# Optimization experiments

Hardware: AMD Instinct MI355X
Metric: run time of the kernel (lower is better)

The kernel has to match this reference:

```python
import jax, jax.numpy as jnp
import numpy as np
import math

EMBED = 1024
HEADS = 16
HEAD_DIM = EMBED // HEADS


def setup_inputs() -> dict:
    key = jax.random.key(0)
    k1, k2, k3 = jax.random.split(key, 3)
    B, C, N = 2, EMBED, 2048
    x = jax.random.normal(k1, (B, C, N), dtype=jnp.float32)
    # Conv1d(kernel_size=1, bias=False) weights, stored as [out_ch, in_ch]
    fan = 1.0 / math.sqrt(EMBED)
    w_qkv = jax.random.uniform(k2, (3 * EMBED, EMBED), dtype=jnp.float32, minval=-fan, maxval=fan)
    w_out = jax.random.uniform(k3, (EMBED, EMBED), dtype=jnp.float32, minval=-fan, maxval=fan)
    return {"x": x, "w_qkv": w_qkv, "w_out": w_out}


def reference(x, w_qkv, w_out):
    B, C, N = x.shape
    H, HD = HEADS, HEAD_DIM
    # 1x1 conv == channel matmul: [B, 3E, N]
    qkv = jnp.einsum('oc,bcn->bon', w_qkv, x)
    # permute -> [B, N, 3E]; reshape splits 3E as (H, 3*HD) per original code
    qkv = qkv.transpose(0, 2, 1).reshape(B, N, H, 3 * HD)
    qkv = qkv.transpose(0, 2, 1, 3)  # [B, H, N, 3*HD]
    q, k, v = jnp.split(qkv, 3, axis=-1)  # each [B, H, N, HD]
    scale = 1.0 / math.sqrt(HD)
    scores = jnp.einsum('bhnd,bhmd->bhnm', q, k) * scale
    weight = jax.nn.softmax(scores, axis=-1)
    vals = jnp.einsum('bhnm,bhmd->bhnd', weight, v)
    vals = vals.transpose(0, 2, 1, 3).reshape(B, N, C)  # [B, N, C]
    y = jnp.einsum('oc,bnc->bon', w_out, vals)  # [B, C, N]
    return y
```

## Files before the change

kernel.cpp:

```cpp
#include <hip/hip_runtime.h>
#include <stdint.h>

typedef unsigned short u16;
typedef __attribute__((ext_vector_type(8))) short bf16x8;
typedef __attribute__((ext_vector_type(4))) float f32x4;

#define NSEQ  2048
#define EMBED 1024
#define NHEAD 16
#define HDIM  64
#define QSCALE 0.1803368801111204f

__device__ __forceinline__ u16 f2bf(float f) {
  uint32_t u = __builtin_bit_cast(uint32_t, f);
  u += 0x7fffu + ((u >> 16) & 1u);
  return (u16)(u >> 16);
}

__device__ __forceinline__ uint32_t cvtpk(float a, float b) {
  uint32_t r;
  asm("v_cvt_pk_bf16_f32 %0, %1, %2" : "=v"(r) : "v"(a), "v"(b));
  return r;
}

__device__ __forceinline__ void gl_lds16(const void* g, void* l) {
  __builtin_amdgcn_global_load_lds(
      (const __attribute__((address_space(1))) void*)g,
      (__attribute__((address_space(3))) void*)l, 16, 0, 0);
}

struct alignas(8) us4 { u16 a, b, c, d; };

__global__ __launch_bounds__(256)
void convertw(const float* __restrict__ wq, const float* __restrict__ wo,
              u16* __restrict__ oq, u16* __restrict__ oo) {
  int idx = blockIdx.x * 256 + threadIdx.x;
  const float* src;
  u16* dst;
  if (idx < 786432) { src = wq; dst = oq; }
  else { idx -= 786432; src = wo; dst = oo; }
  f32x4 v = ((const f32x4*)src)[idx];
  us4 r;
  r.a = f2bf(v[0]); r.b = f2bf(v[1]); r.c = f2bf(v[2]); r.d = f2bf(v[3]);
  ((us4*)dst)[idx] = r;
}

__global__ __launch_bounds__(256)
void transpose_x(const float* __restrict__ x, u16* __restrict__ xT) {
  __shared__ float tile[32][33];
  const int b = blockIdx.z;
  const int n0 = blockIdx.x * 32, c0 = blockIdx.y * 32;
  const int tx = threadIdx.x & 31, ty = threadIdx.x >> 5;
  const float* xb = x + (size_t)b * EMBED * NSEQ;
  #pragma unroll
  for (int k = 0; k < 4; ++k)
    tile[ty + k * 8][tx] = xb[(size_t)(c0 + ty + k * 8) * NSEQ + n0 + tx];
  __syncthreads();
  u16* xTb = xT + (size_t)b * NSEQ * EMBED;
  #pragma unroll
  for (int k = 0; k < 4; ++k)
    xTb[(size_t)(n0 + ty + k * 8) * EMBED + c0 + tx] = f2bf(tile[tx][ty + k * 8]);
}

template<int EPI, int MR>
__global__ __launch_bounds__(256, 2)
void gemm_bt(const u16* __restrict__ A, const u16* __restrict__ Bm,
             u16* __restrict__ o_q, u16* __restrict__ o_k, u16* __restrict__ o_vt,
             float* __restrict__ o_f)
{
  __shared__ u16 lA[MR * 32 * 64];
  __shared__ u16 lB[128 * 64];
  const int t  = threadIdx.x;
  const int w  = t >> 6;
  const int l  = t & 63;
  const int lr = l & 15, lh = l >> 4;
  const int wm = w >> 1, wn = w & 1;
  const int bz = blockIdx.z;
  const int NT  = (EPI == 0 ? 384 : 256);
  const int c   = blockIdx.x + 16 * blockIdx.y;
  const int swz = (c & 7) * (NT / 8) + (c >> 3);
  const int m0  = (swz & 15) * (MR * 32);
  const int n0  = (swz >> 4) * 128;

  const u16* Ab = A  + (EPI == 0 ? (size_t)bz * NSEQ * EMBED : (size_t)0);
  const u16* Bb = Bm + (EPI == 0 ? (size_t)0 : (size_t)bz * NSEQ * EMBED);

  f32x4 acc[MR][4];
  #pragma unroll
  for (int i = 0; i < MR; ++i)
    #pragma unroll
    for (int j = 0; j < 4; ++j)
      acc[i][j] = (f32x4){0.f, 0.f, 0.f, 0.f};

  const int srow = t >> 3;
  const int slot = t & 7;
  char* ldsA = (char*)lA + (w << 10);
  char* ldsB = (char*)lB + (w << 10);

  for (int k0 = 0; k0 < EMBED; k0 += 64) {
    __syncthreads();
    #pragma unroll
    for (int i = 0; i < MR; ++i) {
      const int row = i * 32 + srow;
      const int sc  = ((slot * 16) ^ ((row & 7) << 4)) >> 1;
      gl_lds16(Ab + (size_t)(m0 + row) * EMBED + k0 + sc, ldsA + i * 4096);
    }
    #pragma unroll
    for (int i = 0; i < 4; ++i) {
      const int row = i * 32 + srow;
      const int sc  = ((slot * 16) ^ ((row & 7) << 4)) >> 1;
      gl_lds16(Bb + (size_t)(n0 + row) * EMBED + k0 + sc, ldsB + i * 4096);
    }
    __syncthreads();
    #pragma unroll
    for (int kk = 0; kk < 2; ++kk) {
      bf16x8 af[MR], bfr[4];
      #pragma unroll
      for (int mr = 0; mr < MR; ++mr) {
        const int row = wm * (MR * 16) + mr * 16 + lr;
        const int c2  = (kk * 64 + lh * 16) ^ ((row & 7) << 4);
        af[mr] = *(const bf16x8*)((const char*)lA + row * 128 + c2);
      }
      #pragma unroll
      for (int nc = 0; nc < 4; ++nc) {
        const int row = wn * 64 + nc * 16 + lr;
        const int c2  = (kk * 64 + lh * 16) ^ ((row & 7) << 4);
        bfr[nc] = *(const bf16x8*)((const char*)lB + row * 128 + c2);
      }
      #pragma unroll
      for (int mr = 0; mr < MR; ++mr)
        #pragma unroll
        for (int nc = 0; nc < 4; ++nc)
          acc[mr][nc] = __builtin_amdgcn_mfma_f32_16x16x32_bf16(
              af[mr], bfr[nc], acc[mr][nc], 0, 0, 0);
    }
  }

  if constexpr (EPI == 0) {
    #pragma unroll
    for (int mr = 0; mr < MR; ++mr) {
      #pragma unroll
      for (int nc = 0; nc < 4; ++nc) {
        const int o  = n0 + wn * 64 + nc * 16 + lr;
        const int h  = o / 192;
        const int rr = o - h * 192;
        const size_t bh = (size_t)bz * NHEAD + h;
        #pragma unroll
        for (int r = 0; r < 4; ++r) {
          const int n = m0 + wm * (MR * 16) + mr * 16 + lh * 4 + r;
          if (rr < 64)       o_q [(bh * NSEQ + n) * HDIM + rr]         = f2bf(acc[mr][nc][r] * QSCALE);
          else if (rr < 128) o_k [(bh * NSEQ + n) * HDIM + (rr - 64)]  = f2bf(acc[mr][nc][r]);
          else               o_vt[(bh * HDIM + (rr - 128)) * NSEQ + n] = f2bf(acc[mr][nc][r]);
        }
      }
    }
  } else {
    #pragma unroll
    for (int mr = 0; mr < MR; ++mr)
      #pragma unroll
      for (int nc = 0; nc < 4; ++nc)
        #pragma unroll
        for (int r = 0; r < 4; ++r) {
          const int o = m0 + wm * (MR * 16) + mr * 16 + lh * 4 + r;
          const int n = n0 + wn * 64 + nc * 16 + lr;
          o_f[((size_t)bz * EMBED + o) * NSEQ + n] = acc[mr][nc][r];
        }
  }
}

__global__ __launch_bounds__(256, 4)
void attn(const u16* __restrict__ Q, const u16* __restrict__ K,
          const u16* __restrict__ Vt, u16* __restrict__ vals)
{
  __shared__ u16 lK[2][64 * 64], lV[2][64 * 64], lQP[64 * 64];
  const int t  = threadIdx.x;
  const int w  = t >> 6, l = t & 63;
  const int lr = l & 15, lh = l >> 4;
  const int bid = blockIdx.x;
  const int s   = bid >> 3;
  const int bh  = (bid & 7) + 8 * (s >> 5);
  const int q0  = (s & 31) * 64;
  const int b  = bh >> 4, h = bh & 15;
  const size_t qk0 = (size_t)bh * NSEQ * HDIM;
  const size_t vt0 = (size_t)bh * HDIM * NSEQ;
  const int srow = t >> 3, slot = t & 7;
  const int swzr = (lr & 7) << 4;
  char* const pbase = (char*)lQP + (w << 11) + lr * 128;

#define STAGE(J, KB, VB) do {                                                  \
    _Pragma("unroll")                                                          \
    for (int i_ = 0; i_ < 2; ++i_) {                                           \
      const int row_ = i_ * 32 + srow;                                         \
      const int sc_  = ((slot * 16) ^ ((row_ & 7) << 4)) >> 1;                 \
      gl_lds16(K  + qk0 + (size_t)((J) + row_) * HDIM + sc_,                   \
               (char*)(KB) + i_ * 4096 + (w << 10));                           \
      gl_lds16(Vt + vt0 + (size_t)row_ * NSEQ + (J) + sc_,                     \
               (char*)(VB) + i_ * 4096 + (w << 10));                           \
    }                                                                          \
  } while (0)

#define ATILE(KB, VB) do {                                                     \
    f32x4 accS[4];                                                             \
    _Pragma("unroll")                                                          \
    for (int f_ = 0; f_ < 4; ++f_) accS[f_] = (f32x4){0.f, 0.f, 0.f, 0.f};     \
    __builtin_amdgcn_s_setprio(1);                                             \
    _Pragma("unroll")                                                          \
    for (int kk_ = 0; kk_ < 2; ++kk_)                                          \
      _Pragma("unroll")                                                        \
      for (int f_ = 0; f_ < 4; ++f_) {                                         \
        const int row_ = f_ * 16 + lr;                                         \
        const int c2_  = (kk_ * 64 + lh * 16) ^ swzr;                          \
        bf16x8 kf_ = *(const bf16x8*)((const char*)(KB) + row_ * 128 + c2_);   \
        accS[f_] = __builtin_amdgcn_mfma_f32_16x16x32_bf16(kf_, qf[kk_],       \
                                                           accS[f_], 0, 0, 0);\
      }                                                                        \
    __builtin_amdgcn_s_setprio(0);                                             \
    float fm0_ = fmaxf(fmaxf(accS[0][0], accS[0][1]), fmaxf(accS[0][2], accS[0][3])); \
    float fm1_ = fmaxf(fmaxf(accS[1][0], accS[1][1]), fmaxf(accS[1][2], accS[1][3])); \
    float fm2_ = fmaxf(fmaxf(accS[2][0], accS[2][1]), fmaxf(accS[2][2], accS[2][3])); \
    float fm3_ = fmaxf(fmaxf(accS[3][0], accS[3][1]), fmaxf(accS[3][2], accS[3][3])); \
    float tm_ = fmaxf(fmaxf(fm0_, fm1_), fmaxf(fm2_, fm3_));                   \
    tm_ = fmaxf(tm_, __shfl_xor(tm_, 16, 64));                                 \
    tm_ = fmaxf(tm_, __shfl_xor(tm_, 32, 64));                                 \
    if (tm_ > m + 8.f) {            \
      const float al_ = exp2f(m - tm_);                                        \
      lsum *= al_;                                                             \
      _Pragma("unroll")                                                        \
      for (int fd_ = 0; fd_ < 4; ++fd_)                                        \
        _Pragma("unroll")                                                      \
        for (int r_ = 0; r_ < 4; ++r_) accO[fd_][r_] *= al_;                   \
      m = tm_;                                                                 \
    }                                                                          \
    _Pragma("unroll")                                                          \
    for (int f_ = 0; f_ < 4; ++f_) {                                           \
      const float e0_ = exp2f(accS[f_][0] - m);                                \
      const float e1_ = exp2f(accS[f_][1] - m);                                \
      const float e2_ = exp2f(accS[f_][2] - m);                                \
      const float e3_ = exp2f(accS[f_][3] - m);                                \
      lsum += (e0_ + e1_) + (e2_ + e3_);   \
      uint2 pw_;                                                               \
      pw_.x = cvtpk(e0_, e1_);                                                 \
      pw_.y = cvtpk(e2_, e3_);                                                 \
      *(uint2*)(pbase + ((f_ * 32 + lh * 8) ^ swzr)) = pw_;                    \
    }                                                                          \
    __builtin_amdgcn_s_setprio(1);                                             \
    _Pragma("unroll")                                                          \
    for (int kk_ = 0; kk_ < 2; ++kk_) {                                        \
      bf16x8 pf_ = *(const bf16x8*)(pbase + ((kk_ * 64 + lh * 16) ^ swzr));    \
      _Pragma("unroll")                                                        \
      for (int fd_ = 0; fd_ < 4; ++fd_) {                                      \
        const int row_ = fd_ * 16 + lr;                                        \
        const int c2_  = (kk_ * 64 + lh * 16) ^ swzr;                          \
        bf16x8 vf_ = *(const bf16x8*)((const char*)(VB) + row_ * 128 + c2_);   \
        accO[fd_] = __builtin_amdgcn_mfma_f32_16x16x32_bf16(vf_, pf_,          \
                                                            accO[fd_], 0, 0, 0);\
      }                                                                        \
    }                                                                          \
    __builtin_amdgcn_s_setprio(0);                                             \
  } while (0)

  #pragma unroll
  for (int i = 0; i < 2; ++i) {
    const int row = i * 32 + srow;
    const int sc  = ((slot * 16) ^ ((row & 7) << 4)) >> 1;
    gl_lds16(Q + qk0 + (size_t)(q0 + row) * HDIM + sc,
             (char*)lQP + i * 4096 + (w << 10));
  }
  STAGE(0, lK[0], lV[0]);
  STAGE(64, lK[1], lV[1]);
  __syncthreads();

  bf16x8 qf[2];
  {
    const int qrow = w * 16 + lr;
    #pragma unroll
    for (int kk = 0; kk < 2; ++kk)
      qf[kk] = *(const bf16x8*)((const char*)lQP + qrow * 128 +
                                ((kk * 64 + lh * 16) ^ ((qrow & 7) << 4)));
  }

  f32x4 accO[4];
  #pragma unroll
  for (int i = 0; i < 4; ++i) accO[i] = (f32x4){0.f, 0.f, 0.f, 0.f};
  float m = -1e30f, lsum = 0.f;

  for (int tt = 0; tt < 15; ++tt) {
    const int j0 = tt * 128;
    ATILE(lK[0], lV[0]);
    __syncthreads();
    STAGE(j0 + 128, lK[0], lV[0]);
    ATILE(lK[1], lV[1]);
    __syncthreads();
    STAGE(j0 + 192, lK[1], lV[1]);
  }
  ATILE(lK[0], lV[0]);
  __syncthreads();
  ATILE(lK[1], lV[1]);

  lsum += __shfl_xor(lsum, 16, 64);
  lsum += __shfl_xor(lsum, 32, 64);
  const float rl = 1.0f / lsum;
  const int n = q0 + w * 16 + lr;
  #pragma unroll
  for (int fd = 0; fd < 4; ++fd) {
    uint2 ow;
    ow.x = cvtpk(accO[fd][0] * rl, accO[fd][1] * rl);
    ow.y = cvtpk(accO[fd][2] * rl, accO[fd][3] * rl);
    const int c = h * HDIM + fd * 16 + lh * 4;
    *(uint2*)(vals + ((size_t)b * NSEQ + n) * EMBED + c) = ow;
  }
#undef STAGE
#undef ATILE
}

extern "C" void kernel_launch(void* const* d_in, const int* in_sizes, int n_in,
                              void* d_out, int out_size, void* d_ws, size_t ws_size,
                              hipStream_t stream) {
  const float* x    = (const float*)d_in[0];
  const float* wqkv = (const float*)d_in[1];
  const float* wout = (const float*)d_in[2];
  float* y = (float*)d_out;
  char* ws = (char*)d_ws;

  u16* b_wqkv = (u16*)(ws);
  u16* b_wout = (u16*)(ws + 6291456);
  u16* b_xT   = (u16*)(ws + 8388608);
  u16* b_Q    = (u16*)(ws + 16777216);
  u16* b_K    = (u16*)(ws + 25165824);
  u16* b_Vt   = (u16*)(ws + 33554432);
  u16* b_vals = (u16*)(ws + 41943040);

  convertw<<<4096, 256, 0, stream>>>(wqkv, wout, b_wqkv, b_wout);
  transpose_x<<<dim3(64, 32, 2), 256, 0, stream>>>(x, b_xT);
  gemm_bt<0, 4><<<dim3(16, 24, 2), 256, 0, stream>>>(b_xT, b_wqkv, b_Q, b_K, b_Vt, nullptr);
  attn<<<1024, 256, 0, stream>>>(b_Q, b_K, b_Vt, b_vals);
  gemm_bt<1, 2><<<dim3(16, 16, 2), 256, 0, stream>>>(b_wout, b_vals, nullptr, nullptr, nullptr, y);
}
```

Baseline: 200.2 us.

## Precompute LDS addresses, use raw v_exp_f32, wave-uniform rescale, raise GEMM occupancy

After: 189.1 us. 5.5% less time.

```diff
diff --git a/kernel.cpp b/kernel.cpp
--- a/kernel.cpp
+++ b/kernel.cpp
@@ -20,6 +20,12 @@
 __device__ __forceinline__ uint32_t cvtpk(float a, float b) {
   uint32_t r;
   asm("v_cvt_pk_bf16_f32 %0, %1, %2" : "=v"(r) : "v"(a), "v"(b));
+  return r;
+}
+
+__device__ __forceinline__ float ex2f(float x) {
+  float r;
+  asm("v_exp_f32 %0, %1" : "=v"(r) : "v"(x));
   return r;
 }
 
@@ -63,7 +69,7 @@
 }
 
 template<int EPI, int MR>
-__global__ __launch_bounds__(256, 2)
+__global__ __launch_bounds__(256, (MR == 4 ? 3 : 4))
 void gemm_bt(const u16* __restrict__ A, const u16* __restrict__ Bm,
              u16* __restrict__ o_q, u16* __restrict__ o_k, u16* __restrict__ o_vt,
              float* __restrict__ o_f)
@@ -94,39 +100,38 @@
 
   const int srow = t >> 3;
   const int slot = t & 7;
-  char* ldsA = (char*)lA + (w << 10);
-  char* ldsB = (char*)lB + (w << 10);
-
-  for (int k0 = 0; k0 < EMBED; k0 += 64) {
+  const int sc   = ((slot * 16) ^ ((srow & 7) << 4)) >> 1;
+  const int swzr = (lr & 7) << 4;
+
+  const char* aRd0 = (const char*)lA + (wm * (MR * 16) + lr) * 128 + ((lh * 16) ^ swzr);
+  const char* aRd1 = (const char*)lA + (wm * (MR * 16) + lr) * 128 + ((64 + lh * 16) ^ swzr);
+  const char* bRd0 = (const char*)lB + (wn * 64 + lr) * 128 + ((lh * 16) ^ swzr);
+  const char* bRd1 = (const char*)lB + (wn * 64 + lr) * 128 + ((64 + lh * 16) ^ swzr);
+  char* const aDst = (char*)lA + (w << 10);
+  char* const bDst = (char*)lB + (w << 10);
+  const u16* aP = Ab + (size_t)(m0 + srow) * EMBED + sc;
+  const u16* bP = Bb + (size_t)(n0 + srow) * EMBED + sc;
+
+  for (int k0 = 0; k0 < 16; ++k0) {
     __syncthreads();
     #pragma unroll
-    for (int i = 0; i < MR; ++i) {
-      const int row = i * 32 + srow;
-      const int sc  = ((slot * 16) ^ ((row & 7) << 4)) >> 1;
-      gl_lds16(Ab + (size_t)(m0 + row) * EMBED + k0 + sc, ldsA + i * 4096);
-    }
-    #pragma unroll
-    for (int i = 0; i < 4; ++i) {
-      const int row = i * 32 + srow;
-      const int sc  = ((slot * 16) ^ ((row & 7) << 4)) >> 1;
-      gl_lds16(Bb + (size_t)(n0 + row) * EMBED + k0 + sc, ldsB + i * 4096);
-    }
+    for (int i = 0; i < MR; ++i)
+      gl_lds16(aP + (size_t)i * 32 * EMBED, aDst + i * 4096);
+    #pragma unroll
+    for (int i = 0; i < 4; ++i)
+      gl_lds16(bP + (size_t)i * 32 * EMBED, bDst + i * 4096);
     __syncthreads();
     #pragma unroll
     for (int kk = 0; kk < 2; ++kk) {
+      const char* aRk = kk ? aRd1 : aRd0;
+      const char* bRk = kk ? bRd1 : bRd0;
       bf16x8 af[MR], bfr[4];
       #pragma unroll
-      for (int mr = 0; mr < MR; ++mr) {
-        const int row = wm * (MR * 16) + mr * 16 + lr;
-        const int c2  = (kk * 64 + lh * 16) ^ ((row & 7) << 4);
-        af[mr] = *(const bf16x8*)((const char*)lA + row * 128 + c2);
-      }
-      #pragma unroll
-      for (int nc = 0; nc < 4; ++nc) {
-        const int row = wn * 64 + nc * 16 + lr;
-        const int c2  = (kk * 64 + lh * 16) ^ ((row & 7) << 4);
-        bfr[nc] = *(const bf16x8*)((const char*)lB + row * 128 + c2);
-      }
+      for (int mr = 0; mr < MR; ++mr)
+        af[mr] = *(const bf16x8*)(aRk + mr * 2048);
+      #pragma unroll
+      for (int nc = 0; nc < 4; ++nc)
+        bfr[nc] = *(const bf16x8*)(bRk + nc * 2048);
       #pragma unroll
       for (int mr = 0; mr < MR; ++mr)
         #pragma unroll
@@ -134,6 +139,7 @@
           acc[mr][nc] = __builtin_amdgcn_mfma_f32_16x16x32_bf16(
               af[mr], bfr[nc], acc[mr][nc], 0, 0, 0);
     }
+    aP += 64; bP += 64;
   }
 
   if constexpr (EPI == 0) {
@@ -172,7 +178,7 @@
 void attn(const u16* __restrict__ Q, const u16* __restrict__ K,
           const u16* __restrict__ Vt, u16* __restrict__ vals)
 {
-  __shared__ u16 lK[2][64 * 64], lV[2][64 * 64], lQP[64 * 64];
+  __shared__ u16 sm[5 * 64 * 64];
   const int t  = threadIdx.x;
   const int w  = t >> 6, l = t & 63;
   const int lr = l & 15, lh = l >> 4;
@@ -184,36 +190,47 @@
   const size_t qk0 = (size_t)bh * NSEQ * HDIM;
   const size_t vt0 = (size_t)bh * HDIM * NSEQ;
   const int srow = t >> 3, slot = t & 7;
+  const int sc   = ((slot * 16) ^ ((srow & 7) << 4)) >> 1;
   const int swzr = (lr & 7) << 4;
-  char* const pbase = (char*)lQP + (w << 11) + lr * 128;
-
-#define STAGE(J, KB, VB) do {                                                  \
+
+  char* const smB  = (char*)sm;
+  char* const stD  = smB + (w << 10);
+  const char* kv0  = smB + lr * 128 + ((lh * 16) ^ swzr);
+  const char* kv1  = smB + lr * 128 + ((64 + lh * 16) ^ swzr);
+  const char* kvp0 = kv0 + 32768 + (w << 11);
+  const char* kvp1 = kv1 + 32768 + (w << 11);
+  char* const pwb  = smB + 32768 + (w << 11) + lr * 128;
+  char* const pw_[4] = { pwb + ((0 + lh * 8) ^ swzr),  pwb + ((32 + lh * 8) ^ swzr),
+                         pwb + ((64 + lh * 8) ^ swzr),  pwb + ((96 + lh * 8) ^ swzr) };
+
+  const u16* kP = K  + qk0 + (size_t)srow * HDIM + sc;
+  const u16* vP = Vt + vt0 + (size_t)srow * NSEQ + sc;
+
+#define STAGE(KOFF, VOFF, TB) do {                                             \
     _Pragma("unroll")                                                          \
     for (int i_ = 0; i_ < 2; ++i_) {                                           \
-      const int row_ = i_ * 32 + srow;                                         \
-      const int sc_  = ((slot * 16) ^ ((row_ & 7) << 4)) >> 1;                 \
-      gl_lds16(K  + qk0 + (size_t)((J) + row_) * HDIM + sc_,                   \
-               (char*)(KB) + i_ * 4096 + (w << 10));                           \
-      gl_lds16(Vt + vt0 + (size_t)row_ * NSEQ + (J) + sc_,                     \
-               (char*)(VB) + i_ * 4096 + (w << 10));                           \
+      gl_lds16(kP + (KOFF) + (size_t)i_ * 32 * HDIM,                           \
+               stD + (TB) * 8192 + i_ * 4096);                                 \
+      gl_lds16(vP + (VOFF) + (size_t)i_ * 32 * NSEQ,                           \
+               stD + 16384 + (TB) * 8192 + i_ * 4096);                         \
     }                                                                          \
   } while (0)
 
-#define ATILE(KB, VB) do {                                                     \
+#define ATILE(TB) do {                                                         \
     f32x4 accS[4];                                                             \
     _Pragma("unroll")                                                          \
     for (int f_ = 0; f_ < 4; ++f_) accS[f_] = (f32x4){0.f, 0.f, 0.f, 0.f};     \
     __builtin_amdgcn_s_setprio(1);                                             \
     _Pragma("unroll")                                                          \
-    for (int kk_ = 0; kk_ < 2; ++kk_)                                          \
+    for (int kk_ = 0; kk_ < 2; ++kk_) {                                        \
+      const char* kvk_ = kk_ ? kv1 : kv0;                                      \
       _Pragma("unroll")                                                        \
       for (int f_ = 0; f_ < 4; ++f_) {                                         \
-        const int row_ = f_ * 16 + lr;                                         \
-        const int c2_  = (kk_ * 64 + lh * 16) ^ swzr;                          \
-        bf16x8 kf_ = *(const bf16x8*)((const char*)(KB) + row_ * 128 + c2_);   \
+        bf16x8 kf_ = *(const bf16x8*)(kvk_ + (TB) * 8192 + f_ * 2048);         \
         accS[f_] = __builtin_amdgcn_mfma_f32_16x16x32_bf16(kf_, qf[kk_],       \
                                                            accS[f_], 0, 0, 0);\
       }                                                                        \
+    }                                                                          \
     __builtin_amdgcn_s_setprio(0);                                             \
     float fm0_ = fmaxf(fmaxf(accS[0][0], accS[0][1]), fmaxf(accS[0][2], accS[0][3])); \
     float fm1_ = fmaxf(fmaxf(accS[1][0], accS[1][1]), fmaxf(accS[1][2], accS[1][3])); \
@@ -222,36 +239,36 @@
     float tm_ = fmaxf(fmaxf(fm0_, fm1_), fmaxf(fm2_, fm3_));                   \
     tm_ = fmaxf(tm_, __shfl_xor(tm_, 16, 64));                                 \
     tm_ = fmaxf(tm_, __shfl_xor(tm_, 32, 64));                                 \
-    if (tm_ > m + 8.f) {            \
-      const float al_ = exp2f(m - tm_);                                        \
+    if (__any(tm_ - m > 8.f)) {                    \
+      const float nm_ = fmaxf(m, tm_);                                         \
+      const float al_ = ex2f(m - nm_);         \
       lsum *= al_;                                                             \
       _Pragma("unroll")                                                        \
       for (int fd_ = 0; fd_ < 4; ++fd_)                                        \
         _Pragma("unroll")                                                      \
         for (int r_ = 0; r_ < 4; ++r_) accO[fd_][r_] *= al_;                   \
-      m = tm_;                                                                 \
+      m = nm_;                                                                 \
     }                                                                          \
     _Pragma("unroll")                                                          \
     for (int f_ = 0; f_ < 4; ++f_) {                                           \
-      const float e0_ = exp2f(accS[f_][0] - m);                                \
-      const float e1_ = exp2f(accS[f_][1] - m);                                \
-      const float e2_ = exp2f(accS[f_][2] - m);                                \
-      const float e3_ = exp2f(accS[f_][3] - m);                                \
-      lsum += (e0_ + e1_) + (e2_ + e3_);   \
-      uint2 pw_;                                                               \
-      pw_.x = cvtpk(e0_, e1_);                                                 \
-      pw_.y = cvtpk(e2_, e3_);                                                 \
-      *(uint2*)(pbase + ((f_ * 32 + lh * 8) ^ swzr)) = pw_;                    \
+      const float e0_ = ex2f(accS[f_][0] - m);                                 \
+      const float e1_ = ex2f(accS[f_][1] - m);                                 \
+      const float e2_ = ex2f(accS[f_][2] - m);                                 \
+      const float e3_ = ex2f(accS[f_][3] - m);                                 \
+      lsum += (e0_ + e1_) + (e2_ + e3_);                 \
+      uint2 pw_v;                                                              \
+      pw_v.x = cvtpk(e0_, e1_);                                                \
+      pw_v.y = cvtpk(e2_, e3_);                                                \
+      *(uint2*)(pw_[f_]) = pw_v;                                               \
     }                                                                          \
     __builtin_amdgcn_s_setprio(1);                                             \
     _Pragma("unroll")                                                          \
     for (int kk_ = 0; kk_ < 2; ++kk_) {                                        \
-      bf16x8 pf_ = *(const bf16x8*)(pbase + ((kk_ * 64 + lh * 16) ^ swzr));    \
+      const char* kvk_ = kk_ ? kv1 : kv0;                                      \
+      bf16x8 pf_ = *(const bf16x8*)(kk_ ? kvp1 : kvp0);                        \
       _Pragma("unroll")                                                        \
       for (int fd_ = 0; fd_ < 4; ++fd_) {                                      \
-        const int row_ = fd_ * 16 + lr;                                        \
-        const int c2_  = (kk_ * 64 + lh * 16) ^ swzr;                          \
-        bf16x8 vf_ = *(const bf16x8*)((const char*)(VB) + row_ * 128 + c2_);   \
+        bf16x8 vf_ = *(const bf16x8*)(kvk_ + 16384 + (TB) * 8192 + fd_ * 2048);\
         accO[fd_] = __builtin_amdgcn_mfma_f32_16x16x32_bf16(vf_, pf_,          \
                                                             accO[fd_], 0, 0, 0);\
       }                                                                        \
@@ -260,24 +277,17 @@
   } while (0)
 
   #pragma unroll
-  for (int i = 0; i < 2; ++i) {
-    const int row = i * 32 + srow;
-    const int sc  = ((slot * 16) ^ ((row & 7) << 4)) >> 1;
-    gl_lds16(Q + qk0 + (size_t)(q0 + row) * HDIM + sc,
-             (char*)lQP + i * 4096 + (w << 10));
-  }
-  STAGE(0, lK[0], lV[0]);
-  STAGE(64, lK[1], lV[1]);
+  for (int i = 0; i < 2; ++i)
+    gl_lds16(Q + qk0 + (size_t)(q0 + i * 32 + srow) * HDIM + sc,
+             stD + 32768 + i * 4096);
+  STAGE(0, 0, 0);
+  STAGE(64 * HDIM, 64, 1);
+  kP += 128 * HDIM; vP += 128;
   __syncthreads();
 
   bf16x8 qf[2];
-  {
-    const int qrow = w * 16 + lr;
-    #pragma unroll
-    for (int kk = 0; kk < 2; ++kk)
-      qf[kk] = *(const bf16x8*)((const char*)lQP + qrow * 128 +
-                                ((kk * 64 + lh * 16) ^ ((qrow & 7) << 4)));
-  }
+  qf[0] = *(const bf16x8*)kvp0;
+  qf[1] = *(const bf16x8*)kvp1;
 
   f32x4 accO[4];
   #pragma unroll
@@ -285,17 +295,17 @@
   float m = -1e30f, lsum = 0.f;
 
   for (int tt = 0; tt < 15; ++tt) {
-    const int j0 = tt * 128;
-    ATILE(lK[0], lV[0]);
+    ATILE(0);
     __syncthreads();
-    STAGE(j0 + 128, lK[0], lV[0]);
-    ATILE(lK[1], lV[1]);
+    STAGE(0, 0, 0);
+    ATILE(1);
     __syncthreads();
-    STAGE(j0 + 192, lK[1], lV[1]);
+    STAGE(64 * HDIM, 64, 1);
+    kP += 128 * HDIM; vP += 128;
   }
-  ATILE(lK[0], lV[0]);
+  ATILE(0);
   __syncthreads();
-  ATILE(lK[1], lV[1]);
+  ATILE(1);
 
   lsum += __shfl_xor(lsum, 16, 64);
   lsum += __shfl_xor(lsum, 32, 64);
```
